# Performance work log

Measured on AMD Instinct MI355X. Metric: run time of the kernel, lower is better.

## Reference

```python
import jax, jax.numpy as jnp
import numpy as np

B, N_HEADS, D_MODEL, S = 4, 16, 128, 2048
SQRT_D = np.sqrt(D_MODEL).astype(np.float32)


def setup_inputs() -> dict:
    key = jax.random.key(0)
    kx, kq, kk, kv, kw = jax.random.split(key, 5)
    N = B * N_HEADS
    return {
        "x": jax.random.normal(kx, (B, D_MODEL, S), dtype=jnp.float32),
        "Q": jax.random.normal(kq, (N, D_MODEL, S), dtype=jnp.float32),
        "K": jax.random.normal(kk, (N, D_MODEL, S), dtype=jnp.float32),
        "V": jax.random.normal(kv, (N, D_MODEL, S), dtype=jnp.float32),
        "W": jax.random.normal(kw, (N_HEADS * D_MODEL, D_MODEL), dtype=jnp.float32) * 0.02,
    }


def reference(x, Q, K, V, W):
    # x contributes only its shape (the repeated copy is overwritten in the original)
    b, d_model, s = x.shape
    # scores[n, i, j] = sum_d Q[n, d, i] * K[n, d, j] / sqrt(d_model)
    scores = jnp.einsum("ndi,ndj->nij", Q, K) / SQRT_D  # [N, S, S]
    # legacy F.softmax (no dim) on a 3D tensor -> softmax over dim=1 (query index)
    attn = jax.nn.softmax(scores, axis=1)
    # out[n, d, j] = sum_i V[n, d, i] * attn[n, i, j]
    out = jnp.einsum("ndi,nij->ndj", V, attn)  # [N, d_model, S]
    out = out.reshape(b, N_HEADS * d_model, s)  # [B, H*d_model, S]
    # final projection: W^T @ out, W: [H*d_model, d_model]
    return jnp.einsum("hd,bhs->bds", W, out)  # [B, d_model, S]
```

## Files before the change

### kernel.cpp

```cpp
#include <hip/hip_runtime.h>
#include <hip/hip_bf16.h>

typedef unsigned short u16;
typedef unsigned int   u32;
typedef short  short8v __attribute__((ext_vector_type(8)));
typedef u16    u16x8   __attribute__((ext_vector_type(8)));
typedef float  f32x16  __attribute__((ext_vector_type(16)));
typedef float  f32x4v  __attribute__((ext_vector_type(4)));
typedef u32    u32x2   __attribute__((ext_vector_type(2)));
typedef u32    u32x4   __attribute__((ext_vector_type(4)));

#define HEADS 64
#define DMODEL 128
#define SEQ 2048

#define SCQ 0.1275293f


__device__ __forceinline__ f32x16 mfma_bf16(short8v a, short8v b, f32x16 c) {
  return __builtin_amdgcn_mfma_f32_32x32x16_bf16(a, b, c, 0, 0, 0);
}

__device__ __forceinline__ f32x16 fzero16() {
  f32x16 z;
#pragma unroll
  for (int i = 0; i < 16; ++i) z[i] = 0.f;
  return z;
}

__device__ __forceinline__ float fast_exp2(float x) {
  float r;
  asm("v_exp_f32 %0, %1" : "=v"(r) : "v"(x));
  return r;
}

__device__ __forceinline__ u32 bfround(float x) {
  u32 u = __builtin_bit_cast(u32, x);
  u += 0x7fffu + ((u >> 16) & 1u);
  return u >> 16;
}
__device__ __forceinline__ u32 bfpair(float lo, float hi) {
  u32 a = __builtin_bit_cast(u32, lo); a += 0x7fffu + ((a >> 16) & 1u);
  u32 b = __builtin_bit_cast(u32, hi); b += 0x7fffu + ((b >> 16) & 1u);
  return (a >> 16) | (b & 0xffff0000u);
}
__device__ __forceinline__ u32 packbf(float lo, float hi) {
  u32 l16 = (u32)__builtin_bit_cast(u16, __float2bfloat16(lo));
  u32 h16 = (u32)__builtin_bit_cast(u16, __float2bfloat16(hi));
  return l16 | (h16 << 16);
}

typedef const __attribute__((address_space(1))) void* gp1_t;
typedef __attribute__((address_space(3))) void* lp3_t;
__device__ __forceinline__ void gload16(const u16* g, u16* l) {
  __builtin_amdgcn_global_load_lds((gp1_t)g, (lp3_t)l, 16, 0, 0);
}

__device__ __forceinline__ void stage_T(const float* __restrict__ src, int pos0,
                                        u16* lds, int tid) {
  int ic = tid & 7;
  int d0 = (tid >> 3) * 2;
  const float* p = src + d0 * SEQ + pos0 + ic * 8;
  f32x4v xa = *reinterpret_cast<const f32x4v*>(p);
  f32x4v xb = *reinterpret_cast<const f32x4v*>(p + 4);
  f32x4v ya = *reinterpret_cast<const f32x4v*>(p + SEQ);
  f32x4v yb = *reinterpret_cast<const f32x4v*>(p + SEQ + 4);
  u32* lds32 = reinterpret_cast<u32*>(lds);
  int cc = d0 >> 3;
#pragma unroll
  for (int k = 0; k < 8; ++k) {
    int r = ic * 8 + k;
    int c2 = cc ^ (r & 15);
    float xv = (k < 4) ? xa[k & 3] : xb[k & 3];
    float yv = (k < 4) ? ya[k & 3] : yb[k & 3];
    lds32[(r * 128 + c2 * 8 + (d0 & 7)) >> 1] = bfpair(xv, yv);
  }
}

__device__ __forceinline__ short8v ld_at(const u16* lds, int row, int chunk) {
  return *reinterpret_cast<const short8v*>(lds + row * 128 + ((chunk ^ (row & 15)) * 8));
}
__device__ __forceinline__ short8v ld_vt(const u16* lds, int d, int chunk) {
  return *reinterpret_cast<const short8v*>(lds + d * 64 + ((chunk ^ (d & 7)) * 8));
}


__global__ __launch_bounds__(256) void prep_qt(const float* __restrict__ Q,
                                               u16* __restrict__ Qt) {
  int blk = blockIdx.x;
  int n = blk >> 5, pt = blk & 31;
  const float* src = Q + (size_t)n * DMODEL * SEQ;
  u16* dst = Qt + (size_t)n * SEQ * DMODEL + (size_t)pt * 64 * DMODEL;
  int t = threadIdx.x;
  int pq = t & 15, dq = t >> 4;
#pragma unroll
  for (int p = 0; p < 2; ++p) {
    int d0 = (dq + 16 * p) * 4;
    const float* s0 = src + (size_t)d0 * SEQ + pt * 64 + pq * 4;
    f32x4v r0 = *reinterpret_cast<const f32x4v*>(s0);
    f32x4v r1 = *reinterpret_cast<const f32x4v*>(s0 + SEQ);
    f32x4v r2 = *reinterpret_cast<const f32x4v*>(s0 + 2 * SEQ);
    f32x4v r3 = *reinterpret_cast<const f32x4v*>(s0 + 3 * SEQ);
#pragma unroll
    for (int j = 0; j < 4; ++j) {
      u32x2 v = { bfpair(r0[j] * SCQ, r1[j] * SCQ), bfpair(r2[j] * SCQ, r3[j] * SCQ) };
      *reinterpret_cast<u32x2*>(dst + (pq * 4 + j) * DMODEL + d0) = v;
    }
  }
}

__global__ __launch_bounds__(256) void prep_v(const float* __restrict__ V,
                                              u16* __restrict__ V16t) {
  int blk = blockIdx.x;
  int n = blk >> 5, it = blk & 31;
  int t = threadIdx.x;
  int s8 = (t & 7) * 8;
  const float* src = V + (size_t)n * DMODEL * SEQ + it * 64 + s8;
  u16* dst = V16t + (size_t)blk * DMODEL * 64 + s8;
#pragma unroll
  for (int rr = 0; rr < 4; ++rr) {
    int d = (t >> 3) + 32 * rr;
    const float* p = src + (size_t)d * SEQ;
    f32x4v a = *reinterpret_cast<const f32x4v*>(p);
    f32x4v b = *reinterpret_cast<const f32x4v*>(p + 4);
    u32x4 v = { bfpair(a[0], a[1]), bfpair(a[2], a[3]),
                bfpair(b[0], b[1]), bfpair(b[2], b[3]) };
    *reinterpret_cast<u32x4*>(dst + d * 64) = v;
  }
}

__global__ void wtrans_kernel(const float* __restrict__ Wsrc, u16* __restrict__ Wt) {
  int e = blockIdx.x * 256 + threadIdx.x;
#pragma unroll
  for (int rr = 0; rr < 2; ++rr) {
    int o = e + rr * 131072;
    int dm = o >> 11, c = o & 2047;
    Wt[o] = (u16)bfround(Wsrc[c * 128 + dm]);
  }
}

__global__ __launch_bounds__(1024, 4) void attn_kernel(
    const u16* __restrict__ Qt, const float* __restrict__ K,
    const u16* __restrict__ V16t, u16* __restrict__ Ows) {
  __shared__ __align__(16) u16 AT2[2][64 * DMODEL];
  __shared__ __align__(16) u16 VT2[2][DMODEL * 64];
  __shared__ __align__(16) u16 PB[2][256 * 64];
  __shared__ float AL[2][256];
  __shared__ float LL[256];
  const int tid = threadIdx.x;
  const int w = tid >> 6;
  const int lane = tid & 63;
  const int g = lane >> 5;
  const int lj = lane & 31;
  const int p_ = blockIdx.x;
  const int n = ((p_ >> 6) << 3) | (p_ & 7);
  const int j0 = ((p_ >> 3) & 7) * 256;
  const u16* Qtn = Qt + (size_t)n * SEQ * DMODEL;
  const float* Kb = K + (size_t)n * DMODEL * SEQ;
  const u16* Vtn = V16t + (size_t)n * 32 * DMODEL * 64;

  int qoff[2], voff[2];
#pragma unroll
  for (int i = 0; i < 2; ++i) {
    int idx = (w & 7) * 2 + i;
    int pos = idx * 4 + (lane >> 4);
    qoff[i] = pos * DMODEL + (((lane & 15) ^ (pos & 15)) * 8);
    int d = idx * 8 + (lane >> 3);
    voff[i] = d * 64 + (((lane & 7) ^ (d & 7)) * 8);
  }

  if (w < 8) {
    const u16* qb = Qtn;
#pragma unroll
    for (int i = 0; i < 2; ++i)
      gload16(qb + qoff[i], AT2[0] + ((w & 7) * 2 + i) * 512);
  }
  short8v bq[8];
  u16* KS = PB[0];
#pragma unroll 1
  for (int p = 0; p < 4; ++p) {
    if (tid < 512) stage_T(Kb, j0 + p * 64, KS, tid);
    __syncthreads();
    if (w < 8 && (w >> 1) == p) {
      int row = (w & 1) * 32 + lj;
#pragma unroll
      for (int c = 0; c < 8; ++c) bq[c] = ld_at(KS, row, 2 * c + g);
    }
    __syncthreads();
  }

  if (w < 8) {
    float m_run = -1e30f, l_run = 0.f;
    const int prow = w * 32 + lj;
    u16* const prowbase0 = PB[0] + prow * 64;
    u16* const prowbase1 = PB[1] + prow * 64;
    const int swz = prow & 7;

#pragma unroll 1
    for (int t = 0; t <= 32; ++t) {
      if (t < 32) {
        const u16* qb = Qtn + (size_t)((t + 1) & 31) * (64 * DMODEL);
        u16* ab = AT2[(t + 1) & 1];
#pragma unroll
        for (int i = 0; i < 2; ++i)
          gload16(qb + qoff[i], ab + ((w & 7) * 2 + i) * 512);

        const u16* curAT = AT2[t & 1];
        f32x16 c0 = fzero16(), c1 = fzero16();
        __builtin_amdgcn_s_setprio(1);
#pragma unroll
        for (int dc = 0; dc < 8; ++dc) {
          short8v a0 = ld_at(curAT, lj, 2 * dc + g);
          short8v a1 = ld_at(curAT, 32 + lj, 2 * dc + g);
          c0 = mfma_bf16(a0, bq[dc], c0);
          c1 = mfma_bf16(a1, bq[dc], c1);
        }
        __builtin_amdgcn_s_setprio(0);

        float m8[8];
#pragma unroll
        for (int r = 0; r < 8; ++r)
          m8[r] = fmaxf(fmaxf(c0[r], c0[r + 8]), fmaxf(c1[r], c1[r + 8]));
#pragma unroll
        for (int r = 0; r < 4; ++r) m8[r] = fmaxf(m8[r], m8[r + 4]);
        float mx = fmaxf(fmaxf(m8[0], m8[1]), fmaxf(m8[2], m8[3]));
        mx = fmaxf(mx, __shfl_xor(mx, 32, 64));

        float al = 1.0f;
        if (!__all(mx <= m_run + 8.f)) {
          float mn = fmaxf(m_run, mx);
          al = fast_exp2(m_run - mn);
          m_run = mn;
          l_run *= al;
        }
        if (!g) AL[t & 1][prow] = al;

#pragma unroll
        for (int r = 0; r < 16; ++r) c0[r] = fast_exp2(c0[r] - m_run);
#pragma unroll
        for (int r = 0; r < 16; ++r) c1[r] = fast_exp2(c1[r] - m_run);
        float s8[8];
#pragma unroll
        for (int r = 0; r < 8; ++r) s8[r] = (c0[r] + c0[r + 8]) + (c1[r] + c1[r + 8]);
#pragma unroll
        for (int r = 0; r < 4; ++r) s8[r] += s8[r + 4];
        float ps = (s8[0] + s8[1]) + (s8[2] + s8[3]);
        ps += __shfl_xor(ps, 32, 64);
        l_run += ps;

        u16* pdst = (t & 1) ? prowbase1 : prowbase0;
#pragma unroll
        for (int half = 0; half < 2; ++half) {
#pragma unroll
          for (int q = 0; q < 4; ++q) {
            u32x2 val;
            val.x = half ? packbf(c1[4 * q + 0], c1[4 * q + 1])
                         : packbf(c0[4 * q + 0], c0[4 * q + 1]);
            val.y = half ? packbf(c1[4 * q + 2], c1[4 * q + 3])
                         : packbf(c0[4 * q + 2], c0[4 * q + 3]);
            int G = q + 4 * half;
            *reinterpret_cast<u32x2*>(pdst + ((G ^ swz) << 3) + 4 * g) = val;
          }
        }
      }
      __syncthreads();
    }
    if (!g) LL[prow] = l_run;
    __syncthreads();
  } else {
    f32x16 o0 = fzero16(), o1 = fzero16(), o2 = fzero16(), o3 = fzero16();
    const int prow = (w - 8) * 32 + lj;
    const int swz = prow & 7;

#pragma unroll 1
    for (int t = 0; t <= 32; ++t) {
      if (t < 32) {
        const u16* vb = Vtn + (size_t)t * (DMODEL * 64);
        u16* vbuf = VT2[t & 1];
#pragma unroll
        for (int i = 0; i < 2; ++i)
          gload16(vb + voff[i], vbuf + ((w & 7) * 2 + i) * 512);
      }
      if (t >= 1) {
        const int tp = t - 1;
        const u16* curVT = VT2[tp & 1];
        const u16* prowp = PB[tp & 1] + prow * 64;
        float al = AL[tp & 1][prow];
        if (!__all(al == 1.0f)) {
#pragma unroll
          for (int r = 0; r < 16; ++r) { o0[r] *= al; o1[r] *= al; o2[r] *= al; o3[r] *= al; }
        }
        __builtin_amdgcn_s_setprio(1);
#pragma unroll
        for (int kc = 0; kc < 4; ++kc) {
          short8v pf = *reinterpret_cast<const short8v*>(
              prowp + (((2 * kc + g) ^ swz) << 3));
          short8v v0 = ld_vt(curVT, lj,      2 * kc + g);
          short8v v1 = ld_vt(curVT, 32 + lj, 2 * kc + g);
          short8v v2 = ld_vt(curVT, 64 + lj, 2 * kc + g);
          short8v v3 = ld_vt(curVT, 96 + lj, 2 * kc + g);
          o0 = mfma_bf16(v0, pf, o0);
          o1 = mfma_bf16(v1, pf, o1);
          o2 = mfma_bf16(v2, pf, o2);
          o3 = mfma_bf16(v3, pf, o3);
        }
        __builtin_amdgcn_s_setprio(0);
      }
      __syncthreads();
    }
    __syncthreads();
    float inv = 1.f / LL[prow];
    int jme = j0 + prow;
    u16* obase = Ows + ((size_t)n * SEQ + jme) * DMODEL;
#define STORE_OT(OV, DT)                                                  \
    {                                                                     \
      _Pragma("unroll") for (int q = 0; q < 4; ++q) {                     \
        int d0 = (DT) * 32 + 4 * g + 8 * q;                               \
        u32x2 val;                                                        \
        val.x = bfpair(OV[4 * q + 0] * inv, OV[4 * q + 1] * inv);         \
        val.y = bfpair(OV[4 * q + 2] * inv, OV[4 * q + 3] * inv);         \
        *reinterpret_cast<u32x2*>(obase + d0) = val;                      \
      }                                                                   \
    }
    STORE_OT(o0, 0) STORE_OT(o1, 1) STORE_OT(o2, 2) STORE_OT(o3, 3)
#undef STORE_OT
  }
}

__global__ __launch_bounds__(256) void proj_kernel(
    const u16* __restrict__ Ows, const u16* __restrict__ Wt, float* __restrict__ out) {
  __shared__ __align__(16) u16 BT[32 * 128];
  const int tid = threadIdx.x;
  const int w = tid >> 6, lane = tid & 63, g = lane >> 5, lj = lane & 31;
  const int b = blockIdx.x >> 6;
  const int j0 = (blockIdx.x & 63) * 32;
  f32x16 acc = fzero16();
#pragma unroll 1
  for (int h = 0; h < 16; ++h) {
    __syncthreads();
#pragma unroll
    for (int rr = 0; rr < 2; ++rr) {
      int s = tid + rr * 256;
      int r = s >> 4, cc = s & 15;
      u16x8 v = *reinterpret_cast<const u16x8*>(
          Ows + ((size_t)(b * 16 + h) * SEQ + j0 + r) * DMODEL + cc * 8);
      *reinterpret_cast<u16x8*>(BT + r * 128 + ((cc ^ (r & 7)) * 8)) = v;
    }
    __syncthreads();
#pragma unroll
    for (int kc = 0; kc < 8; ++kc) {
      short8v a = *reinterpret_cast<const short8v*>(
          Wt + (size_t)(w * 32 + lj) * SEQ + h * 128 + kc * 16 + g * 8);
      short8v bb = *reinterpret_cast<const short8v*>(
          BT + lj * 128 + (((2 * kc + g) ^ (lj & 7)) * 8));
      acc = mfma_bf16(a, bb, acc);
    }
  }
#pragma unroll
  for (int q = 0; q < 4; ++q) {
#pragma unroll
    for (int r = 0; r < 4; ++r) {
      int dm = w * 32 + 4 * g + 8 * q + r;
      out[((size_t)b * DMODEL + dm) * SEQ + j0 + lj] = acc[4 * q + r];
    }
  }
}

extern "C" void kernel_launch(void* const* d_in, const int* in_sizes, int n_in,
                              void* d_out, int out_size, void* d_ws, size_t ws_size,
                              hipStream_t stream) {
  (void)in_sizes; (void)n_in; (void)out_size; (void)ws_size;
  const float* Q = (const float*)d_in[1];
  const float* K = (const float*)d_in[2];
  const float* V = (const float*)d_in[3];
  const float* W = (const float*)d_in[4];
  const size_t NEL = (size_t)HEADS * SEQ * DMODEL;
  u16* Qt   = (u16*)d_ws;
  u16* V16t = Qt + NEL;
  u16* Ows  = V16t + NEL;
  u16* Wt   = Ows + NEL;
  float* out = (float*)d_out;

  prep_qt<<<dim3(2048), dim3(256), 0, stream>>>(Q, Qt);
  prep_v<<<dim3(2048), dim3(256), 0, stream>>>(V, V16t);
  wtrans_kernel<<<dim3(512), dim3(256), 0, stream>>>(W, Wt);
  attn_kernel<<<dim3(512), dim3(1024), 0, stream>>>(Qt, K, V16t, Ows);
  proj_kernel<<<dim3(256), dim3(256), 0, stream>>>(Ows, Wt, out);
}
```

Before: 238.5 us.

## Rebalance attention warp split: 4 score warps with 32-row query tiles

The attention kernel changes from 8 score warps plus 8 PV warps at 1024 threads to 4 score warps plus 8 PV warps at 768 threads. Each score warp now holds two 32-column K fragments and reuses one Q fragment load across two MFMAs, running two independent online-softmax states. The query tile shrinks from 64 to 32 rows, so the loop runs 64 iterations. V is re-laid out into 32-wide tiles with a new swizzle, and LDS use drops. The aim is less LDS traffic per MFMA and higher occupancy, at the cost of twice as many block barriers and a heavier per-warp softmax load.

```diff
diff --git a/kernel.cpp b/kernel.cpp
--- a/kernel.cpp
+++ b/kernel.cpp
@@ -80,8 +80,9 @@
 __device__ __forceinline__ short8v ld_at(const u16* lds, int row, int chunk) {
   return *reinterpret_cast<const short8v*>(lds + row * 128 + ((chunk ^ (row & 15)) * 8));
 }
-__device__ __forceinline__ short8v ld_vt(const u16* lds, int d, int chunk) {
-  return *reinterpret_cast<const short8v*>(lds + d * 64 + ((chunk ^ (d & 7)) * 8));
+__device__ __forceinline__ short8v ld_vt32(const u16* lds, int d, int ch) {
+  return *reinterpret_cast<const short8v*>(
+      lds + d * 32 + (((ch ^ ((d ^ (d >> 2)) & 3)) & 3) * 8));
 }
 
 
@@ -112,20 +113,20 @@
 __global__ __launch_bounds__(256) void prep_v(const float* __restrict__ V,
                                               u16* __restrict__ V16t) {
   int blk = blockIdx.x;
-  int n = blk >> 5, it = blk & 31;
+  int n = blk >> 5, tp = blk & 31;
   int t = threadIdx.x;
-  int s8 = (t & 7) * 8;
-  const float* src = V + (size_t)n * DMODEL * SEQ + it * 64 + s8;
-  u16* dst = V16t + (size_t)blk * DMODEL * 64 + s8;
-#pragma unroll
-  for (int rr = 0; rr < 4; ++rr) {
-    int d = (t >> 3) + 32 * rr;
-    const float* p = src + (size_t)d * SEQ;
-    f32x4v a = *reinterpret_cast<const f32x4v*>(p);
-    f32x4v b = *reinterpret_cast<const f32x4v*>(p + 4);
+  int tile = tp * 2 + (t >> 7);
+  int d = t & 127;
+  const float* src = V + ((size_t)n * DMODEL + d) * SEQ + tile * 32;
+  u16* dst = V16t + (((size_t)n * 64 + tile) * DMODEL + d) * 32;
+  u32x4* dst16 = reinterpret_cast<u32x4*>(dst);
+#pragma unroll
+  for (int c = 0; c < 4; ++c) {
+    f32x4v a = *reinterpret_cast<const f32x4v*>(src + c * 8);
+    f32x4v b = *reinterpret_cast<const f32x4v*>(src + c * 8 + 4);
     u32x4 v = { bfpair(a[0], a[1]), bfpair(a[2], a[3]),
                 bfpair(b[0], b[1]), bfpair(b[2], b[3]) };
-    *reinterpret_cast<u32x4*>(dst + d * 64) = v;
+    dst16[c] = v;
   }
 }
 
@@ -139,12 +140,12 @@
   }
 }
 
-__global__ __launch_bounds__(1024, 4) void attn_kernel(
+__global__ __launch_bounds__(768, 6) void attn_kernel(
     const u16* __restrict__ Qt, const float* __restrict__ K,
     const u16* __restrict__ V16t, u16* __restrict__ Ows) {
-  __shared__ __align__(16) u16 AT2[2][64 * DMODEL];
-  __shared__ __align__(16) u16 VT2[2][DMODEL * 64];
-  __shared__ __align__(16) u16 PB[2][256 * 64];
+  __shared__ __align__(16) u16 AT2[2][32 * DMODEL];
+  __shared__ __align__(16) u16 VT2[2][DMODEL * 32];
+  __shared__ __align__(16) u16 PB[2][256 * 32];
   __shared__ float AL[2][256];
   __shared__ float LL[256];
   const int tid = threadIdx.x;
@@ -157,134 +158,153 @@
   const int j0 = ((p_ >> 3) & 7) * 256;
   const u16* Qtn = Qt + (size_t)n * SEQ * DMODEL;
   const float* Kb = K + (size_t)n * DMODEL * SEQ;
-  const u16* Vtn = V16t + (size_t)n * 32 * DMODEL * 64;
-
-  int qoff[2], voff[2];
+  const u16* Vtn = V16t + (size_t)n * 64 * DMODEL * 32;
+
+  int qoff[2];
 #pragma unroll
   for (int i = 0; i < 2; ++i) {
-    int idx = (w & 7) * 2 + i;
+    int idx = (w & 3) * 2 + i;
     int pos = idx * 4 + (lane >> 4);
     qoff[i] = pos * DMODEL + (((lane & 15) ^ (pos & 15)) * 8);
-    int d = idx * 8 + (lane >> 3);
-    voff[i] = d * 64 + (((lane & 7) ^ (d & 7)) * 8);
-  }
-
-  if (w < 8) {
-    const u16* qb = Qtn;
+  }
+  int voff;
+  {
+    int idx = (w - 4) & 7;
+    int d = idx * 16 + (lane >> 2);
+    voff = d * 32 + ((((lane & 3) ^ ((d ^ (d >> 2)) & 3)) & 3) * 8);
+  }
+
+  if (w < 4) {
 #pragma unroll
     for (int i = 0; i < 2; ++i)
-      gload16(qb + qoff[i], AT2[0] + ((w & 7) * 2 + i) * 512);
-  }
-  short8v bq[8];
-  u16* KS = PB[0];
+      gload16(Qtn + qoff[i], AT2[0] + ((w & 3) * 2 + i) * 512);
+  }
+
+  short8v bq0[8], bq1[8];
+  u16* KS = &PB[0][0];
 #pragma unroll 1
   for (int p = 0; p < 4; ++p) {
     if (tid < 512) stage_T(Kb, j0 + p * 64, KS, tid);
     __syncthreads();
-    if (w < 8 && (w >> 1) == p) {
+    if (w < 4) {
       int row = (w & 1) * 32 + lj;
-#pragma unroll
-      for (int c = 0; c < 8; ++c) bq[c] = ld_at(KS, row, 2 * c + g);
-    }
-    __syncthreads();
-  }
-
-  if (w < 8) {
-    float m_run = -1e30f, l_run = 0.f;
-    const int prow = w * 32 + lj;
-    u16* const prowbase0 = PB[0] + prow * 64;
-    u16* const prowbase1 = PB[1] + prow * 64;
-    const int swz = prow & 7;
+      if ((w >> 1) == p) {
+#pragma unroll
+        for (int c = 0; c < 8; ++c) bq0[c] = ld_at(KS, row, 2 * c + g);
+      }
+      if ((w >> 1) + 2 == p) {
+#pragma unroll
+        for (int c = 0; c < 8; ++c) bq1[c] = ld_at(KS, row, 2 * c + g);
+      }
+    }
+    __syncthreads();
+  }
+
+  if (w < 4) {
+    float m_a = -1e30f, l_a = 0.f, m_b = -1e30f, l_b = 0.f;
+    const int ja = w * 32 + lj;
+    const int jb = 128 + w * 32 + lj;
+    const int swza = (ja ^ (ja >> 2)) & 3;
+    const int swzb = (jb ^ (jb >> 2)) & 3;
 
 #pragma unroll 1
-    for (int t = 0; t <= 32; ++t) {
-      if (t < 32) {
-        const u16* qb = Qtn + (size_t)((t + 1) & 31) * (64 * DMODEL);
+    for (int t = 0; t <= 64; ++t) {
+      if (t < 64) {
+        const u16* qb = Qtn + (size_t)((t + 1) & 63) * (32 * DMODEL);
         u16* ab = AT2[(t + 1) & 1];
 #pragma unroll
         for (int i = 0; i < 2; ++i)
-          gload16(qb + qoff[i], ab + ((w & 7) * 2 + i) * 512);
+          gload16(qb + qoff[i], ab + ((w & 3) * 2 + i) * 512);
 
         const u16* curAT = AT2[t & 1];
-        f32x16 c0 = fzero16(), c1 = fzero16();
+        f32x16 ca = fzero16(), cb = fzero16();
         __builtin_amdgcn_s_setprio(1);
 #pragma unroll
         for (int dc = 0; dc < 8; ++dc) {
-          short8v a0 = ld_at(curAT, lj, 2 * dc + g);
-          short8v a1 = ld_at(curAT, 32 + lj, 2 * dc + g);
-          c0 = mfma_bf16(a0, bq[dc], c0);
-          c1 = mfma_bf16(a1, bq[dc], c1);
+          short8v a = ld_at(curAT, lj, 2 * dc + g);
+          ca = mfma_bf16(a, bq0[dc], ca);
+          cb = mfma_bf16(a, bq1[dc], cb);
         }
         __builtin_amdgcn_s_setprio(0);
 
-        float m8[8];
-#pragma unroll
-        for (int r = 0; r < 8; ++r)
-          m8[r] = fmaxf(fmaxf(c0[r], c0[r + 8]), fmaxf(c1[r], c1[r + 8]));
-#pragma unroll
-        for (int r = 0; r < 4; ++r) m8[r] = fmaxf(m8[r], m8[r + 4]);
-        float mx = fmaxf(fmaxf(m8[0], m8[1]), fmaxf(m8[2], m8[3]));
-        mx = fmaxf(mx, __shfl_xor(mx, 32, 64));
-
-        float al = 1.0f;
-        if (!__all(mx <= m_run + 8.f)) {
-          float mn = fmaxf(m_run, mx);
-          al = fast_exp2(m_run - mn);
-          m_run = mn;
-          l_run *= al;
-        }
-        if (!g) AL[t & 1][prow] = al;
-
-#pragma unroll
-        for (int r = 0; r < 16; ++r) c0[r] = fast_exp2(c0[r] - m_run);
-#pragma unroll
-        for (int r = 0; r < 16; ++r) c1[r] = fast_exp2(c1[r] - m_run);
-        float s8[8];
-#pragma unroll
-        for (int r = 0; r < 8; ++r) s8[r] = (c0[r] + c0[r + 8]) + (c1[r] + c1[r + 8]);
-#pragma unroll
-        for (int r = 0; r < 4; ++r) s8[r] += s8[r + 4];
-        float ps = (s8[0] + s8[1]) + (s8[2] + s8[3]);
-        ps += __shfl_xor(ps, 32, 64);
-        l_run += ps;
-
-        u16* pdst = (t & 1) ? prowbase1 : prowbase0;
-#pragma unroll
-        for (int half = 0; half < 2; ++half) {
-#pragma unroll
-          for (int q = 0; q < 4; ++q) {
-            u32x2 val;
-            val.x = half ? packbf(c1[4 * q + 0], c1[4 * q + 1])
-                         : packbf(c0[4 * q + 0], c0[4 * q + 1]);
-            val.y = half ? packbf(c1[4 * q + 2], c1[4 * q + 3])
-                         : packbf(c0[4 * q + 2], c0[4 * q + 3]);
-            int G = q + 4 * half;
-            *reinterpret_cast<u32x2*>(pdst + ((G ^ swz) << 3) + 4 * g) = val;
-          }
+        float t8[8];
+#pragma unroll
+        for (int r = 0; r < 8; ++r) t8[r] = fmaxf(ca[r], ca[r + 8]);
+#pragma unroll
+        for (int r = 0; r < 4; ++r) t8[r] = fmaxf(t8[r], t8[r + 4]);
+        float mxa = fmaxf(fmaxf(t8[0], t8[1]), fmaxf(t8[2], t8[3]));
+        mxa = fmaxf(mxa, __shfl_xor(mxa, 32, 64));
+        float ala = 1.0f;
+        if (!__all(mxa <= m_a + 8.f)) {
+          float mn = fmaxf(m_a, mxa);
+          ala = fast_exp2(m_a - mn);
+          m_a = mn; l_a *= ala;
+        }
+#pragma unroll
+        for (int r = 0; r < 16; ++r) ca[r] = fast_exp2(ca[r] - m_a);
+#pragma unroll
+        for (int r = 0; r < 8; ++r) t8[r] = ca[r] + ca[r + 8];
+#pragma unroll
+        for (int r = 0; r < 4; ++r) t8[r] += t8[r + 4];
+        float psa = (t8[0] + t8[1]) + (t8[2] + t8[3]);
+        psa += __shfl_xor(psa, 32, 64);
+        l_a += psa;
+
+#pragma unroll
+        for (int r = 0; r < 8; ++r) t8[r] = fmaxf(cb[r], cb[r + 8]);
+#pragma unroll
+        for (int r = 0; r < 4; ++r) t8[r] = fmaxf(t8[r], t8[r + 4]);
+        float mxb = fmaxf(fmaxf(t8[0], t8[1]), fmaxf(t8[2], t8[3]));
+        mxb = fmaxf(mxb, __shfl_xor(mxb, 32, 64));
+        float alb = 1.0f;
+        if (!__all(mxb <= m_b + 8.f)) {
+          float mn = fmaxf(m_b, mxb);
+          alb = fast_exp2(m_b - mn);
+          m_b = mn; l_b *= alb;
+        }
+#pragma unroll
+        for (int r = 0; r < 16; ++r) cb[r] = fast_exp2(cb[r] - m_b);
+#pragma unroll
+        for (int r = 0; r < 8; ++r) t8[r] = cb[r] + cb[r + 8];
+#pragma unroll
+        for (int r = 0; r < 4; ++r) t8[r] += t8[r + 4];
+        float psb = (t8[0] + t8[1]) + (t8[2] + t8[3]);
+        psb += __shfl_xor(psb, 32, 64);
+        l_b += psb;
+
+        if (!g) { AL[t & 1][ja] = ala; AL[t & 1][jb] = alb; }
+
+        u16* pb = PB[t & 1];
+        u16* pda = pb + ja * 32;
+        u16* pdb = pb + jb * 32;
+#pragma unroll
+        for (int q = 0; q < 4; ++q) {
+          u32x2 va = { packbf(ca[4 * q + 0], ca[4 * q + 1]),
+                       packbf(ca[4 * q + 2], ca[4 * q + 3]) };
+          *reinterpret_cast<u32x2*>(pda + ((q ^ swza) << 3) + 4 * g) = va;
+          u32x2 vb = { packbf(cb[4 * q + 0], cb[4 * q + 1]),
+                       packbf(cb[4 * q + 2], cb[4 * q + 3]) };
+          *reinterpret_cast<u32x2*>(pdb + ((q ^ swzb) << 3) + 4 * g) = vb;
         }
       }
       __syncthreads();
     }
-    if (!g) LL[prow] = l_run;
+    if (!g) { LL[ja] = l_a; LL[jb] = l_b; }
     __syncthreads();
   } else {
     f32x16 o0 = fzero16(), o1 = fzero16(), o2 = fzero16(), o3 = fzero16();
-    const int prow = (w - 8) * 32 + lj;
-    const int swz = prow & 7;
+    const int prow = (w - 4) * 32 + lj;
+    const int swzp = (prow ^ (prow >> 2)) & 3;
 
 #pragma unroll 1
-    for (int t = 0; t <= 32; ++t) {
-      if (t < 32) {
-        const u16* vb = Vtn + (size_t)t * (DMODEL * 64);
-        u16* vbuf = VT2[t & 1];
-#pragma unroll
-        for (int i = 0; i < 2; ++i)
-          gload16(vb + voff[i], vbuf + ((w & 7) * 2 + i) * 512);
-      }
+    for (int t = 0; t <= 64; ++t) {
+      if (t < 64)
+        gload16(Vtn + (size_t)t * (DMODEL * 32) + voff,
+                VT2[t & 1] + ((w - 4) & 7) * 512);
       if (t >= 1) {
         const int tp = t - 1;
         const u16* curVT = VT2[tp & 1];
-        const u16* prowp = PB[tp & 1] + prow * 64;
+        const u16* pbase = PB[tp & 1] + prow * 32;
         float al = AL[tp & 1][prow];
         if (!__all(al == 1.0f)) {
 #pragma unroll
@@ -292,13 +312,13 @@
         }
         __builtin_amdgcn_s_setprio(1);
 #pragma unroll
-        for (int kc = 0; kc < 4; ++kc) {
+        for (int kc = 0; kc < 2; ++kc) {
           short8v pf = *reinterpret_cast<const short8v*>(
-              prowp + (((2 * kc + g) ^ swz) << 3));
-          short8v v0 = ld_vt(curVT, lj,      2 * kc + g);
-          short8v v1 = ld_vt(curVT, 32 + lj, 2 * kc + g);
-          short8v v2 = ld_vt(curVT, 64 + lj, 2 * kc + g);
-          short8v v3 = ld_vt(curVT, 96 + lj, 2 * kc + g);
+              pbase + (((2 * kc + g) ^ swzp) << 3));
+          short8v v0 = ld_vt32(curVT, lj,      2 * kc + g);
+          short8v v1 = ld_vt32(curVT, 32 + lj, 2 * kc + g);
+          short8v v2 = ld_vt32(curVT, 64 + lj, 2 * kc + g);
+          short8v v3 = ld_vt32(curVT, 96 + lj, 2 * kc + g);
           o0 = mfma_bf16(v0, pf, o0);
           o1 = mfma_bf16(v1, pf, o1);
           o2 = mfma_bf16(v2, pf, o2);
@@ -384,6 +404,6 @@
   prep_qt<<<dim3(2048), dim3(256), 0, stream>>>(Q, Qt);
   prep_v<<<dim3(2048), dim3(256), 0, stream>>>(V, V16t);
   wtrans_kernel<<<dim3(512), dim3(256), 0, stream>>>(W, Wt);
-  attn_kernel<<<dim3(512), dim3(1024), 0, stream>>>(Qt, K, V16t, Ows);
+  attn_kernel<<<dim3(512), dim3(768), 0, stream>>>(Qt, K, V16t, Ows);
   proj_kernel<<<dim3(256), dim3(256), 0, stream>>>(Ows, Wt, out);
 }
```

Result: slower. 644.5 us (+170.2%).
